# Optimization experiments

Measured on AMD Instinct MI355X. Metric: run time of the kernel, lower is better.

Reference implementation:

```python
import jax, jax.numpy as jnp
import numpy as np

DIM = 768
NUM_HEADS = 12
HEAD_DIM = DIM // NUM_HEADS
HIDDEN = int(DIM * 0.5)  # 384, per Block: hidden_features = int(dim * 0.5)
SCALE = HEAD_DIM ** 0.5  # NOTE: source multiplies by sqrt(head_dim) (qk_scale=None path)


def setup_inputs() -> dict:
    key = jax.random.key(0)
    ks = jax.random.split(key, 10)
    s = 0.02
    return {
        "x": jax.random.normal(ks[0], (8, 1024, DIM), dtype=jnp.float32),
        "ln1_w": jnp.ones((DIM,), jnp.float32),
        "ln1_b": jnp.zeros((DIM,), jnp.float32),
        "ln2_w": jnp.ones((DIM,), jnp.float32),
        "ln2_b": jnp.zeros((DIM,), jnp.float32),
        "w_qkv": jax.random.normal(ks[1], (DIM, 3 * DIM), jnp.float32) * s,  # no bias (qkv_bias=None)
        "w_proj": jax.random.normal(ks[2], (DIM, DIM), jnp.float32) * s,    # no bias (qkv_bias=None)
        "w_fc1": jax.random.normal(ks[3], (DIM, HIDDEN), jnp.float32) * s,
        "b_fc1": jnp.zeros((HIDDEN,), jnp.float32),
        "w_fc2": jax.random.normal(ks[4], (HIDDEN, DIM), jnp.float32) * s,
        "b_fc2": jnp.zeros((DIM,), jnp.float32),
    }


def _layernorm(x, w, b, eps=1e-5):
    mu = jnp.mean(x, axis=-1, keepdims=True)
    var = jnp.mean(jnp.square(x - mu), axis=-1, keepdims=True)
    return (x - mu) * jax.lax.rsqrt(var + eps) * w + b


def reference(x, ln1_w, ln1_b, ln2_w, ln2_b, w_qkv, w_proj, w_fc1, b_fc1, w_fc2, b_fc2):
    B, N, C = x.shape
    # --- attention branch (pre-norm) ---
    h = _layernorm(x, ln1_w, ln1_b)
    qkv = h @ w_qkv  # [B,N,3C]
    qkv = qkv.reshape(B, N, 3, NUM_HEADS, HEAD_DIM)
    q = jnp.transpose(qkv[:, :, 0], (0, 2, 1, 3))  # [B,H,N,D]
    k = jnp.transpose(qkv[:, :, 1], (0, 2, 1, 3))
    v = jnp.transpose(qkv[:, :, 2], (0, 2, 1, 3))
    attn = jnp.einsum("bhnd,bhmd->bhnm", q, k) * SCALE
    attn = jax.nn.softmax(attn, axis=-1)
    out = jnp.einsum("bhnm,bhmd->bhnd", attn, v)
    out = jnp.transpose(out, (0, 2, 1, 3)).reshape(B, N, C)
    x = x + out @ w_proj
    # --- MLP branch (pre-norm) ---
    h = _layernorm(x, ln2_w, ln2_b)
    h = jax.nn.gelu(h @ w_fc1 + b_fc1, approximate=False)
    x = x + (h @ w_fc2 + b_fc2)
    return x
```

## Files before the change

kernel.cpp:

```cpp
#include <hip/hip_runtime.h>
#include <hip/hip_bf16.h>
#include <math.h>

#define DIM 768
#define NHEAD 12
#define HD 64
#define HIDDEN 384
#define BATCH 8
#define SEQ 1024
#define ROWS (BATCH*SEQ)
#define CHUNKB 4
#define CHUNKR (CHUNKB*SEQ)

typedef short bf16x8 __attribute__((ext_vector_type(8)));
typedef float f32x4 __attribute__((ext_vector_type(4)));
typedef unsigned int u32x2 __attribute__((ext_vector_type(2)));
typedef unsigned short u16;
typedef unsigned int u32;

__device__ __forceinline__ u16 f2bs(float f) {
    unsigned int u = __float_as_uint(f);
    unsigned int r = (u + 0x7FFFu + ((u >> 16) & 1u)) >> 16;
    return (u16)r;
}

__device__ __forceinline__ u32 packbf2(float a, float b) {
    __hip_bfloat162 h = __float22bfloat162_rn(make_float2(a, b));
    u32 r;
    __builtin_memcpy(&r, &h, 4);
    return r;
}

__device__ __forceinline__ void gld16(const u16* g, u16* l) {
    __builtin_amdgcn_global_load_lds(
        (const __attribute__((address_space(1))) unsigned int*)g,
        (__attribute__((address_space(3))) unsigned int*)l, 16, 0, 0);
}

__global__ __launch_bounds__(256) void wtrans(const float* __restrict__ W,
                                              u16* __restrict__ Wt, int K, int N) {
    __shared__ float tile[32][33];
    int n0 = blockIdx.x * 32, k0 = blockIdx.y * 32;
    int tx = threadIdx.x & 31, ty = threadIdx.x >> 5;
#pragma unroll
    for (int i = 0; i < 4; i++)
        tile[ty + i * 8][tx] = W[(long)(k0 + ty + i * 8) * N + n0 + tx];
    __syncthreads();
#pragma unroll
    for (int i = 0; i < 4; i++)
        Wt[(long)(n0 + ty + i * 8) * K + k0 + tx] = f2bs(tile[tx][ty + i * 8]);
}

__global__ __launch_bounds__(256) void lnorm(const float* __restrict__ X,
                                             const float* __restrict__ w,
                                             const float* __restrict__ b,
                                             u16* __restrict__ Y) {
    int row = blockIdx.x;
    const float* xr = X + (long)row * DIM;
    int t = threadIdx.x;
    float v0 = xr[t], v1 = xr[t + 256], v2 = xr[t + 512];
    float s = v0 + v1 + v2;
    float s2 = v0 * v0 + v1 * v1 + v2 * v2;
    for (int off = 1; off < 64; off <<= 1) {
        s  += __shfl_xor(s,  off, 64);
        s2 += __shfl_xor(s2, off, 64);
    }
    __shared__ float ss[4], ss2[4];
    int wid = t >> 6;
    if ((t & 63) == 0) { ss[wid] = s; ss2[wid] = s2; }
    __syncthreads();
    s  = ss[0] + ss[1] + ss[2] + ss[3];
    s2 = ss2[0] + ss2[1] + ss2[2] + ss2[3];
    float mu = s * (1.0f / DIM);
    float var = s2 * (1.0f / DIM) - mu * mu;
    float rstd = rsqrtf(var + 1e-5f);
    u16* yr = Y + (long)row * DIM;
    yr[t]       = f2bs((v0 - mu) * rstd * w[t]       + b[t]);
    yr[t + 256] = f2bs((v1 - mu) * rstd * w[t + 256] + b[t + 256]);
    yr[t + 512] = f2bs((v2 - mu) * rstd * w[t + 512] + b[t + 512]);
}

template <int BM, int BN, int EPI>
__global__ __launch_bounds__(256) void gemm_bt(const u16* __restrict__ A,
                                               const u16* __restrict__ Bt,
                                               int M, int N, int K,
                                               u16* __restrict__ Cb,
                                               float* __restrict__ Cf,
                                               const float* __restrict__ resid,
                                               const float* __restrict__ bias) {
    constexpr int MB = BM / 32, NB = BN / 32;
    __shared__ u16 As[BM * 64];
    __shared__ u16 Bs[BN * 64];
    int m0 = blockIdx.y * BM;
    int n0 = blockIdx.x * BN;
    int t = threadIdx.x;
    int lane = t & 63, w = t >> 6;
    int quad = lane >> 4, l16 = lane & 15;
    int wr = w >> 1, wc = w & 1;
    int lr = lane >> 3, lc = lane & 7;
    int sc = (lc ^ lr) * 8;
    int x7 = l16 & 7;

    f32x4 acc[MB][NB];
#pragma unroll
    for (int mb = 0; mb < MB; mb++)
#pragma unroll
        for (int nb = 0; nb < NB; nb++) acc[mb][nb] = (f32x4){0.f, 0.f, 0.f, 0.f};

    for (int kt = 0; kt < K; kt += 64) {
        __syncthreads();
#pragma unroll
        for (int i = 0; i < BM / 32; i++) {
            int rb = i * 32 + w * 8;
            gld16(&A[(long)(m0 + rb + lr) * K + kt + sc], &As[rb * 64]);
        }
#pragma unroll
        for (int i = 0; i < BN / 32; i++) {
            int rb = i * 32 + w * 8;
            gld16(&Bt[(long)(n0 + rb + lr) * K + kt + sc], &Bs[rb * 64]);
        }
        __syncthreads();
#pragma unroll
        for (int kh = 0; kh < 2; kh++) {
            bf16x8 af[MB], bfr[NB];
#pragma unroll
            for (int mb = 0; mb < MB; mb++)
                af[mb] = *(const bf16x8*)&As[(wr * (BM / 2) + mb * 16 + l16) * 64 +
                                             (((kh * 4 + quad) ^ x7) * 8)];
#pragma unroll
            for (int nb = 0; nb < NB; nb++)
                bfr[nb] = *(const bf16x8*)&Bs[(wc * (BN / 2) + nb * 16 + l16) * 64 +
                                              (((kh * 4 + quad) ^ x7) * 8)];
#pragma unroll
            for (int mb = 0; mb < MB; mb++)
#pragma unroll
                for (int nb = 0; nb < NB; nb++)
                    acc[mb][nb] = __builtin_amdgcn_mfma_f32_16x16x32_bf16(af[mb], bfr[nb], acc[mb][nb], 0, 0, 0);
        }
    }

    int mbase = m0 + wr * (BM / 2), nbase = n0 + wc * (BN / 2);
#pragma unroll
    for (int mb = 0; mb < MB; mb++)
#pragma unroll
        for (int nb = 0; nb < NB; nb++) {
            int r0 = mbase + mb * 16 + quad * 4;
            int c = nbase + nb * 16 + l16;
#pragma unroll
            for (int r = 0; r < 4; r++) {
                float v = acc[mb][nb][r];
                long idx = (long)(r0 + r) * N + c;
                if (EPI == 0) {
                    Cb[idx] = f2bs(v);
                } else if (EPI == 1) {
                    Cf[idx] = resid[idx] + v;
                } else if (EPI == 2) {
                    float xg = v + bias[c];
                    Cb[idx] = f2bs(xg * 0.5f * (1.0f + erff(xg * 0.70710678118f)));
                } else {
                    Cf[idx] = resid[idx] + v + bias[c];
                }
            }
        }
}

__global__ __launch_bounds__(256, 3) void attn(const u16* __restrict__ QKV, u16* __restrict__ O) {
    __shared__ u16 Ks[128 * 72];
    __shared__ u16 Vs[64 * 136];
    __shared__ u16 Ps[4][16 * 136];
    int q0 = blockIdx.x * 128;
    int h = blockIdx.y;
    int b = blockIdx.z;
    int t = threadIdx.x;
    int lane = t & 63, w = t >> 6;
    int quad = lane >> 4, l16 = lane & 15;

    const long rs = 3 * DIM;
    const u16* base = QKV + (long)b * SEQ * rs;

    bf16x8 qf[2][2];
#pragma unroll
    for (int rg = 0; rg < 2; rg++) {
        int qrow = q0 + w * 32 + rg * 16 + l16;
        qf[rg][0] = *(const bf16x8*)&base[(long)qrow * rs + h * 64 + quad * 8];
        qf[rg][1] = *(const bf16x8*)&base[(long)qrow * rs + h * 64 + 32 + quad * 8];
    }

    f32x4 o[2][4];
#pragma unroll
    for (int rg = 0; rg < 2; rg++)
#pragma unroll
        for (int jb = 0; jb < 4; jb++) o[rg][jb] = (f32x4){0.f, 0.f, 0.f, 0.f};
    float m_run[2] = {-1e30f, -1e30f};
    float l_run[2] = {0.f, 0.f};

    const float L2E8 = 11.54156032f;

    int kvr = t >> 1, khalf = (t & 1) * 32;
    int vp = t & 63, vo = t >> 6;

    const u16* kptr = &base[(long)kvr * rs + DIM + h * 64 + khalf];
    const u16* vptr = &base[(long)(2 * vp) * rs + 2 * DIM + h * 64 + vo * 16];
    const long kstep = (long)128 * rs;

    bf16x8 kpre[4], va0, va1, vb0, vb1;
    kpre[0] = *(const bf16x8*)&kptr[0];
    kpre[1] = *(const bf16x8*)&kptr[8];
    kpre[2] = *(const bf16x8*)&kptr[16];
    kpre[3] = *(const bf16x8*)&kptr[24];
    va0 = *(const bf16x8*)&vptr[0];
    va1 = *(const bf16x8*)&vptr[8];
    vb0 = *(const bf16x8*)&vptr[rs];
    vb1 = *(const bf16x8*)&vptr[rs + 8];

    for (int kt = 0; kt < SEQ; kt += 128) {
        __syncthreads();
        {
            *(bf16x8*)&Ks[kvr * 72 + khalf]      = kpre[0];
            *(bf16x8*)&Ks[kvr * 72 + khalf + 8]  = kpre[1];
            *(bf16x8*)&Ks[kvr * 72 + khalf + 16] = kpre[2];
            *(bf16x8*)&Ks[kvr * 72 + khalf + 24] = kpre[3];
#pragma unroll
            for (int j = 0; j < 8; j++) {
                u32 pk = (u32)(u16)va0[j] | ((u32)(u16)vb0[j] << 16);
                *(u32*)&Vs[(vo * 16 + j) * 136 + 2 * vp] = pk;
            }
#pragma unroll
            for (int j = 0; j < 8; j++) {
                u32 pk = (u32)(u16)va1[j] | ((u32)(u16)vb1[j] << 16);
                *(u32*)&Vs[(vo * 16 + 8 + j) * 136 + 2 * vp] = pk;
            }
        }
        __syncthreads();

        if (kt + 128 < SEQ) {
            kptr += kstep; vptr += kstep;
            kpre[0] = *(const bf16x8*)&kptr[0];
            kpre[1] = *(const bf16x8*)&kptr[8];
            kpre[2] = *(const bf16x8*)&kptr[16];
            kpre[3] = *(const bf16x8*)&kptr[24];
            va0 = *(const bf16x8*)&vptr[0];
            va1 = *(const bf16x8*)&vptr[8];
            vb0 = *(const bf16x8*)&vptr[rs];
            vb1 = *(const bf16x8*)&vptr[rs + 8];
        }

#pragma unroll
        for (int rg = 0; rg < 2; rg++) {
            f32x4 s[8];
#pragma unroll
            for (int jb = 0; jb < 8; jb++) {
                bf16x8 kf0 = *(const bf16x8*)&Ks[(jb * 16 + l16) * 72 + quad * 8];
                bf16x8 kf1 = *(const bf16x8*)&Ks[(jb * 16 + l16) * 72 + 32 + quad * 8];
                f32x4 z = (f32x4){0.f, 0.f, 0.f, 0.f};
                z = __builtin_amdgcn_mfma_f32_16x16x32_bf16(kf0, qf[rg][0], z, 0, 0, 0);
                z = __builtin_amdgcn_mfma_f32_16x16x32_bf16(kf1, qf[rg][1], z, 0, 0, 0);
                s[jb] = z;
            }

            float m1 = s[0][0];
#pragma unroll
            for (int jb = 0; jb < 8; jb++)
#pragma unroll
                for (int r = 0; r < 4; r++) m1 = fmaxf(m1, s[jb][r]);
            m1 = fmaxf(m1, __shfl_xor(m1, 16, 64));
            m1 = fmaxf(m1, __shfl_xor(m1, 32, 64));
            float mn = fmaxf(m_run[rg], m1);
            float alpha = exp2f((m_run[rg] - mn) * L2E8);
            m_run[rg] = mn;
            float mn8 = mn * L2E8;
            float rsum = 0.f;
#pragma unroll
            for (int jb = 0; jb < 8; jb++)
#pragma unroll
                for (int r = 0; r < 4; r++) {
                    float p = exp2f(fmaf(s[jb][r], L2E8, -mn8));
                    s[jb][r] = p;
                    rsum += p;
                }
            rsum += __shfl_xor(rsum, 16, 64);
            rsum += __shfl_xor(rsum, 32, 64);
            l_run[rg] = l_run[rg] * alpha + rsum;

            float a0 = __shfl(alpha, quad * 4 + 0, 16);
            float a1 = __shfl(alpha, quad * 4 + 1, 16);
            float a2 = __shfl(alpha, quad * 4 + 2, 16);
            float a3 = __shfl(alpha, quad * 4 + 3, 16);
#pragma unroll
            for (int jb = 0; jb < 4; jb++) {
                o[rg][jb][0] *= a0; o[rg][jb][1] *= a1;
                o[rg][jb][2] *= a2; o[rg][jb][3] *= a3;
            }

#pragma unroll
            for (int jb = 0; jb < 8; jb++) {
                u32x2 pk;
                pk.x = packbf2(s[jb][0], s[jb][1]);
                pk.y = packbf2(s[jb][2], s[jb][3]);
                *(u32x2*)&Ps[w][l16 * 136 + jb * 16 + quad * 4] = pk;
            }

#pragma unroll
            for (int c = 0; c < 4; c++) {
                bf16x8 pf = *(const bf16x8*)&Ps[w][l16 * 136 + c * 32 + quad * 8];
#pragma unroll
                for (int jb = 0; jb < 4; jb++) {
                    bf16x8 vf = *(const bf16x8*)&Vs[(jb * 16 + l16) * 136 + c * 32 + quad * 8];
                    o[rg][jb] = __builtin_amdgcn_mfma_f32_16x16x32_bf16(pf, vf, o[rg][jb], 0, 0, 0);
                }
            }
        }
    }

#pragma unroll
    for (int rg = 0; rg < 2; rg++) {
        float l0 = __shfl(l_run[rg], quad * 4 + 0, 16);
        float l1 = __shfl(l_run[rg], quad * 4 + 1, 16);
        float l2 = __shfl(l_run[rg], quad * 4 + 2, 16);
        float l3 = __shfl(l_run[rg], quad * 4 + 3, 16);
        u16* orow = O + ((long)(b * SEQ + q0 + w * 32 + rg * 16)) * DIM + h * 64;
#pragma unroll
        for (int jb = 0; jb < 4; jb++) {
            u32 p01 = packbf2(o[rg][jb][0] / l0, o[rg][jb][1] / l1);
            u32 p23 = packbf2(o[rg][jb][2] / l2, o[rg][jb][3] / l3);
            int cidx = jb * 16 + l16;
            orow[(long)(quad * 4 + 0) * DIM + cidx] = (u16)p01;
            orow[(long)(quad * 4 + 1) * DIM + cidx] = (u16)(p01 >> 16);
            orow[(long)(quad * 4 + 2) * DIM + cidx] = (u16)p23;
            orow[(long)(quad * 4 + 3) * DIM + cidx] = (u16)(p23 >> 16);
        }
    }
}

extern "C" void kernel_launch(void* const* d_in, const int* in_sizes, int n_in,
                              void* d_out, int out_size, void* d_ws, size_t ws_size,
                              hipStream_t stream) {
    const float* x     = (const float*)d_in[0];
    const float* ln1w  = (const float*)d_in[1];
    const float* ln1b  = (const float*)d_in[2];
    const float* ln2w  = (const float*)d_in[3];
    const float* ln2b  = (const float*)d_in[4];
    const float* wqkv  = (const float*)d_in[5];
    const float* wproj = (const float*)d_in[6];
    const float* wfc1  = (const float*)d_in[7];
    const float* bfc1  = (const float*)d_in[8];
    const float* wfc2  = (const float*)d_in[9];
    const float* bfc2  = (const float*)d_in[10];
    float* out = (float*)d_out;

    char* ws = (char*)d_ws;
    size_t off = 0;
    auto alloc = [&](size_t bytes) {
        void* p = ws + off;
        off = (off + bytes + 255) & ~(size_t)255;
        return p;
    };
    u16* wt_qkv  = (u16*)alloc((size_t)3 * DIM * DIM * 2);
    u16* wt_proj = (u16*)alloc((size_t)DIM * DIM * 2);
    u16* wt_fc1  = (u16*)alloc((size_t)HIDDEN * DIM * 2);
    u16* wt_fc2  = (u16*)alloc((size_t)DIM * HIDDEN * 2);
    u16* hbuf    = (u16*)alloc((size_t)ROWS * DIM * 2);
    u16* gbuf    = (u16*)alloc((size_t)ROWS * HIDDEN * 2);
    size_t qkv_bytes = (size_t)ROWS * 3 * DIM * 2;
    u16* qkvfull = (off + qkv_bytes + 1024 <= ws_size) ? (u16*)alloc(qkv_bytes) : nullptr;

    wtrans<<<dim3(3 * DIM / 32, DIM / 32), 256, 0, stream>>>(wqkv, wt_qkv, DIM, 3 * DIM);
    wtrans<<<dim3(DIM / 32, DIM / 32), 256, 0, stream>>>(wproj, wt_proj, DIM, DIM);
    wtrans<<<dim3(HIDDEN / 32, DIM / 32), 256, 0, stream>>>(wfc1, wt_fc1, DIM, HIDDEN);
    wtrans<<<dim3(DIM / 32, HIDDEN / 32), 256, 0, stream>>>(wfc2, wt_fc2, HIDDEN, DIM);

    lnorm<<<ROWS, 256, 0, stream>>>(x, ln1w, ln1b, hbuf);

    if (qkvfull) {
        gemm_bt<128, 128, 0><<<dim3(3 * DIM / 128, ROWS / 128), 256, 0, stream>>>(
            hbuf, wt_qkv, ROWS, 3 * DIM, DIM, qkvfull, nullptr, nullptr, nullptr);
        attn<<<dim3(SEQ / 128, NHEAD, BATCH), 256, 0, stream>>>(qkvfull, hbuf);
    } else {
        u16* qd = (u16*)d_out;
        for (int c = 0; c < ROWS / CHUNKR; c++) {
            const u16* hA = hbuf + (size_t)c * CHUNKR * DIM;
            gemm_bt<128, 128, 0><<<dim3(3 * DIM / 128, CHUNKR / 128), 256, 0, stream>>>(
                hA, wt_qkv, CHUNKR, 3 * DIM, DIM, qd, nullptr, nullptr, nullptr);
            attn<<<dim3(SEQ / 128, NHEAD, CHUNKB), 256, 0, stream>>>(
                qd, hbuf + (size_t)c * CHUNKR * DIM);
        }
    }

    gemm_bt<128, 64, 1><<<dim3(DIM / 64, ROWS / 128), 256, 0, stream>>>(
        hbuf, wt_proj, ROWS, DIM, DIM, nullptr, out, x, nullptr);

    lnorm<<<ROWS, 256, 0, stream>>>(out, ln2w, ln2b, hbuf);

    gemm_bt<64, 64, 2><<<dim3(HIDDEN / 64, ROWS / 64), 256, 0, stream>>>(
        hbuf, wt_fc1, ROWS, HIDDEN, DIM, gbuf, nullptr, nullptr, bfc1);

    gemm_bt<128, 64, 3><<<dim3(DIM / 64, ROWS / 128), 256, 0, stream>>>(
        gbuf, wt_fc2, ROWS, DIM, HIDDEN, nullptr, out, out, bfc2);
}
```

Measured before the change: 276.1 us.

## Keep P in registers for PV MFMA and skip lazy softmax rescales

The attention kernel drops the shared-memory round trip for the probability tile P. It feeds the packed S accumulators straight into 16x16x16 bf16 MFMAs against V, which frees LDS and allows the launch bound to rise to 4 blocks per SM. It also adds a lazy online-softmax rescale, updating the running max and rescaling O only when any lane's new max exceeds the old one by more than a threshold. This adds a wave-wide branch and uses a smaller-K MFMA variant, and it relies on exp values staying bounded in between rescales.

Result: slower. 327.4 us (+18.6%).

```diff
diff --git a/kernel.cpp b/kernel.cpp
--- a/kernel.cpp
+++ b/kernel.cpp
@@ -13,6 +13,7 @@
 #define CHUNKR (CHUNKB*SEQ)
 
 typedef short bf16x8 __attribute__((ext_vector_type(8)));
+typedef short bf16x4 __attribute__((ext_vector_type(4)));
 typedef float f32x4 __attribute__((ext_vector_type(4)));
 typedef unsigned int u32x2 __attribute__((ext_vector_type(2)));
 typedef unsigned short u16;
@@ -164,10 +165,9 @@
         }
 }
 
-__global__ __launch_bounds__(256, 3) void attn(const u16* __restrict__ QKV, u16* __restrict__ O) {
+__global__ __launch_bounds__(256, 4) void attn(const u16* __restrict__ QKV, u16* __restrict__ O) {
     __shared__ u16 Ks[128 * 72];
     __shared__ u16 Vs[64 * 136];
-    __shared__ u16 Ps[4][16 * 136];
     int q0 = blockIdx.x * 128;
     int h = blockIdx.y;
     int b = blockIdx.z;
@@ -190,7 +190,7 @@
 #pragma unroll
     for (int rg = 0; rg < 2; rg++)
 #pragma unroll
-        for (int jb = 0; jb < 4; jb++) o[rg][jb] = (f32x4){0.f, 0.f, 0.f, 0.f};
+        for (int dt = 0; dt < 4; dt++) o[rg][dt] = (f32x4){0.f, 0.f, 0.f, 0.f};
     float m_run[2] = {-1e30f, -1e30f};
     float l_run[2] = {0.f, 0.f};
 
@@ -265,9 +265,10 @@
                 for (int r = 0; r < 4; r++) m1 = fmaxf(m1, s[jb][r]);
             m1 = fmaxf(m1, __shfl_xor(m1, 16, 64));
             m1 = fmaxf(m1, __shfl_xor(m1, 32, 64));
-            float mn = fmaxf(m_run[rg], m1);
-            float alpha = exp2f((m_run[rg] - mn) * L2E8);
-            m_run[rg] = mn;
+
+            float mn = m_run[rg];
+            int resc = __any(m1 > mn + 1.0f);
+            if (resc) mn = fmaxf(mn, m1);
             float mn8 = mn * L2E8;
             float rsum = 0.f;
 #pragma unroll
@@ -280,33 +281,34 @@
                 }
             rsum += __shfl_xor(rsum, 16, 64);
             rsum += __shfl_xor(rsum, 32, 64);
-            l_run[rg] = l_run[rg] * alpha + rsum;
-
-            float a0 = __shfl(alpha, quad * 4 + 0, 16);
-            float a1 = __shfl(alpha, quad * 4 + 1, 16);
-            float a2 = __shfl(alpha, quad * 4 + 2, 16);
-            float a3 = __shfl(alpha, quad * 4 + 3, 16);
-#pragma unroll
-            for (int jb = 0; jb < 4; jb++) {
-                o[rg][jb][0] *= a0; o[rg][jb][1] *= a1;
-                o[rg][jb][2] *= a2; o[rg][jb][3] *= a3;
+
+            if (resc) {
+                float alpha = exp2f((m_run[rg] - mn) * L2E8);
+                m_run[rg] = mn;
+                float a0 = __shfl(alpha, quad * 4 + 0, 16);
+                float a1 = __shfl(alpha, quad * 4 + 1, 16);
+                float a2 = __shfl(alpha, quad * 4 + 2, 16);
+                float a3 = __shfl(alpha, quad * 4 + 3, 16);
+#pragma unroll
+                for (int dt = 0; dt < 4; dt++) {
+                    o[rg][dt][0] *= a0; o[rg][dt][1] *= a1;
+                    o[rg][dt][2] *= a2; o[rg][dt][3] *= a3;
+                }
+                l_run[rg] = l_run[rg] * alpha + rsum;
+            } else {
+                l_run[rg] += rsum;
             }
 
 #pragma unroll
             for (int jb = 0; jb < 8; jb++) {
-                u32x2 pk;
-                pk.x = packbf2(s[jb][0], s[jb][1]);
-                pk.y = packbf2(s[jb][2], s[jb][3]);
-                *(u32x2*)&Ps[w][l16 * 136 + jb * 16 + quad * 4] = pk;
-            }
-
-#pragma unroll
-            for (int c = 0; c < 4; c++) {
-                bf16x8 pf = *(const bf16x8*)&Ps[w][l16 * 136 + c * 32 + quad * 8];
-#pragma unroll
-                for (int jb = 0; jb < 4; jb++) {
-                    bf16x8 vf = *(const bf16x8*)&Vs[(jb * 16 + l16) * 136 + c * 32 + quad * 8];
-                    o[rg][jb] = __builtin_amdgcn_mfma_f32_16x16x32_bf16(pf, vf, o[rg][jb], 0, 0, 0);
+                union { u32 u[2]; bf16x4 v; } pc;
+                pc.u[0] = packbf2(s[jb][0], s[jb][1]);
+                pc.u[1] = packbf2(s[jb][2], s[jb][3]);
+                bf16x4 pf = pc.v;
+#pragma unroll
+                for (int dt = 0; dt < 4; dt++) {
+                    bf16x4 vf = *(const bf16x4*)&Vs[(dt * 16 + l16) * 136 + jb * 16 + quad * 4];
+                    o[rg][dt] = __builtin_amdgcn_mfma_f32_16x16x16bf16_1k(pf, vf, o[rg][dt], 0, 0, 0);
                 }
             }
         }
@@ -320,10 +322,10 @@
         float l3 = __shfl(l_run[rg], quad * 4 + 3, 16);
         u16* orow = O + ((long)(b * SEQ + q0 + w * 32 + rg * 16)) * DIM + h * 64;
 #pragma unroll
-        for (int jb = 0; jb < 4; jb++) {
-            u32 p01 = packbf2(o[rg][jb][0] / l0, o[rg][jb][1] / l1);
-            u32 p23 = packbf2(o[rg][jb][2] / l2, o[rg][jb][3] / l3);
-            int cidx = jb * 16 + l16;
+        for (int dt = 0; dt < 4; dt++) {
+            u32 p01 = packbf2(o[rg][dt][0] / l0, o[rg][dt][1] / l1);
+            u32 p23 = packbf2(o[rg][dt][2] / l2, o[rg][dt][3] / l3);
+            int cidx = dt * 16 + l16;
             orow[(long)(quad * 4 + 0) * DIM + cidx] = (u16)p01;
             orow[(long)(quad * 4 + 1) * DIM + cidx] = (u16)(p01 >> 16);
             orow[(long)(quad * 4 + 2) * DIM + cidx] = (u16)p23;
```
